# Performance work log

Hardware: AMD Instinct MI355X
Metric: run time of the kernel (lower is better)

The kernel has to match this reference:

```python
import jax, jax.numpy as jnp
import numpy as np

D = 256        # feature dim
H = 8          # num_heads
HD = D // H    # head dim = 32
G = 16         # graphs in batch
NA = 128       # nodes per graph, side A
NB = 128       # nodes per graph, side B


def setup_inputs() -> dict:
    key = jax.random.key(0)
    ks = jax.random.split(key, 7)
    s = 1.0 / np.sqrt(D)
    A = jax.random.normal(ks[0], (G * NA, D), dtype=jnp.float32)
    B = jax.random.normal(ks[1], (G * NB, D), dtype=jnp.float32)
    batch1 = jnp.repeat(jnp.arange(G, dtype=jnp.int64), NA)
    batch2 = jnp.repeat(jnp.arange(G, dtype=jnp.int64), NB)
    W1 = jax.random.normal(ks[2], (D, D), dtype=jnp.float32) * s
    bias1 = jax.random.normal(ks[3], (D,), dtype=jnp.float32) * s
    W2 = jax.random.normal(ks[4], (D, D), dtype=jnp.float32) * s
    bias2 = jax.random.normal(ks[5], (D,), dtype=jnp.float32) * s
    q = jax.random.normal(ks[6], (HD,), dtype=jnp.float32) * s
    return {"A": A, "batch1": batch1, "B": B, "batch2": batch2,
            "W1": W1, "bias1": bias1, "W2": W2, "bias2": bias2, "q": q}


def reference(A, batch1, B, batch2, W1, bias1, W2, bias2, q):
    # equal-size graphs: counts are uniform, so torch.split == reshape
    g = int(np.asarray(batch1)[-1]) + 1
    nA = A.shape[0] // g
    nB = B.shape[0] // g
    x1 = A @ W1.T + bias1            # [g*nA, D]
    x2 = B @ W2.T + bias2            # [g*nB, D]
    # faithful to torch: raw C-order view [nA, D] -> [H, nA, HD]
    x1 = x1.reshape(g, H, nA, HD)    # [g, H, nA, hd]
    x2 = x2.reshape(g, H, nB, HD)    # [g, H, nB, hd]
    # att[g,h,i,j] = sum_k tanh(x1[g,h,i,k] * x2[g,h,j,k]) * q[k]
    att = jnp.einsum('ghijk,k->ghij',
                     jnp.tanh(x1[:, :, :, None, :] * x2[:, :, None, :, :]), q)
    b2a = jax.nn.softmax(att.mean(axis=3), axis=2)   # [g, H, nA]
    a2b = jax.nn.softmax(att.mean(axis=2), axis=2)   # [g, H, nB]
    A_p = jnp.einsum('ghik,ghi->ghk', x1, b2a).reshape(g, D)
    B_p = jnp.einsum('ghjk,ghj->ghk', x2, a2b).reshape(g, D)
    return jnp.concatenate([A_p, B_p], axis=1)       # [g, 2D]
```

## Files before the change

kernel.cpp:

```cpp
#include <hip/hip_runtime.h>

#define C2L2E 2.8853900817779268f
#define LOG2E 1.4426950408889634f

#define WS_X1   0
#define WS_X2   524288
#define WS_X1S  1048576
#define WS_RS   1572864
#define WS_CQ   1589248
#define WS_AH   1703936
#define WS_AL   1966080
#define WS_BH   2228224
#define WS_BL   2490368
#define WS_W1H  2752512
#define WS_W1L  2785280
#define WS_W2H  2818048
#define WS_W2L  2850816

typedef short bf16x8 __attribute__((ext_vector_type(8)));
typedef float f32x4 __attribute__((ext_vector_type(4)));

__device__ __forceinline__ unsigned short bf16rne(float f) {
    unsigned u = __float_as_uint(f);
    u += 0x7FFF + ((u >> 16) & 1);
    return (unsigned short)(u >> 16);
}
__device__ __forceinline__ float bf16tof(unsigned short h) {
    return __uint_as_float(((unsigned)h) << 16);
}
__device__ __forceinline__ float rfl(float x) {
    return __uint_as_float(__builtin_amdgcn_readfirstlane(__float_as_uint(x)));
}

__global__ __launch_bounds__(256) void k0_convert(
        const float* __restrict__ A, const float* __restrict__ B,
        const float* __restrict__ W1, const float* __restrict__ W2,
        float* __restrict__ ws) {
    const int t = blockIdx.x * 256 + threadIdx.x;
    const float* src; unsigned short *dh, *dl; int tl;
    if (t < 65536)       { src = A;  dh = (unsigned short*)(ws + WS_AH);  dl = (unsigned short*)(ws + WS_AL);  tl = t; }
    else if (t < 131072) { src = B;  dh = (unsigned short*)(ws + WS_BH);  dl = (unsigned short*)(ws + WS_BL);  tl = t - 65536; }
    else if (t < 139264) { src = W1; dh = (unsigned short*)(ws + WS_W1H); dl = (unsigned short*)(ws + WS_W1L); tl = t - 131072; }
    else                 { src = W2; dh = (unsigned short*)(ws + WS_W2H); dl = (unsigned short*)(ws + WS_W2L); tl = t - 139264; }
    const int lane = tl & 63, kt = (tl >> 6) & 7, rt = tl >> 9;
    const int row = rt * 16 + (lane & 15);
    const int col = kt * 32 + (lane >> 4) * 8;
    float4 v0 = *(const float4*)(src + (size_t)row * 256 + col);
    float4 v1 = *(const float4*)(src + (size_t)row * 256 + col + 4);
    ushort4 h0, h1, l0, l1;
    h0.x = bf16rne(v0.x); l0.x = bf16rne(v0.x - bf16tof(h0.x));
    h0.y = bf16rne(v0.y); l0.y = bf16rne(v0.y - bf16tof(h0.y));
    h0.z = bf16rne(v0.z); l0.z = bf16rne(v0.z - bf16tof(h0.z));
    h0.w = bf16rne(v0.w); l0.w = bf16rne(v0.w - bf16tof(h0.w));
    h1.x = bf16rne(v1.x); l1.x = bf16rne(v1.x - bf16tof(h1.x));
    h1.y = bf16rne(v1.y); l1.y = bf16rne(v1.y - bf16tof(h1.y));
    h1.z = bf16rne(v1.z); l1.z = bf16rne(v1.z - bf16tof(h1.z));
    h1.w = bf16rne(v1.w); l1.w = bf16rne(v1.w - bf16tof(h1.w));
    ((ushort4*)dh)[tl * 2]     = h0;
    ((ushort4*)dh)[tl * 2 + 1] = h1;
    ((ushort4*)dl)[tl * 2]     = l0;
    ((ushort4*)dl)[tl * 2 + 1] = l1;
}

__global__ __launch_bounds__(256) void k1_mfma(
        const float* __restrict__ b1, const float* __restrict__ b2,
        float* __restrict__ ws) {
    const int bid = blockIdx.x, tid = threadIdx.x;
    const int mat = bid >> 7, idx = bid & 127;
    const int r0 = (idx >> 2) * 64, c0 = (idx & 3) * 64;
    const unsigned short* IH  = (const unsigned short*)(ws + (mat ? WS_BH : WS_AH));
    const unsigned short* IL  = (const unsigned short*)(ws + (mat ? WS_BL : WS_AL));
    const unsigned short* WHp = (const unsigned short*)(ws + (mat ? WS_W2H : WS_W1H));
    const unsigned short* WLp = (const unsigned short*)(ws + (mat ? WS_W2L : WS_W1L));
    const float* bs = mat ? b2 : b1;
    float* xo = ws + (mat ? WS_X2 : WS_X1);

    const int wv = tid >> 6, lane = tid & 63;
    const int rt = (idx >> 2) * 4 + wv;
    const int ct0 = (idx & 3) * 4;

    f32x4 acc[4];
    #pragma unroll
    for (int nt = 0; nt < 4; ++nt) acc[nt] = (f32x4){0.f, 0.f, 0.f, 0.f};

    for (int kt = 0; kt < 8; ++kt) {
        bf16x8 ah = *(const bf16x8*)(IH + ((size_t)(rt * 8 + kt) * 64 + lane) * 8);
        bf16x8 al = *(const bf16x8*)(IL + ((size_t)(rt * 8 + kt) * 64 + lane) * 8);
        #pragma unroll
        for (int nt = 0; nt < 4; ++nt) {
            const int ct = ct0 + nt;
            bf16x8 wh = *(const bf16x8*)(WHp + ((size_t)(ct * 8 + kt) * 64 + lane) * 8);
            bf16x8 wl = *(const bf16x8*)(WLp + ((size_t)(ct * 8 + kt) * 64 + lane) * 8);
            acc[nt] = __builtin_amdgcn_mfma_f32_16x16x32_bf16(ah, wh, acc[nt], 0, 0, 0);
            acc[nt] = __builtin_amdgcn_mfma_f32_16x16x32_bf16(ah, wl, acc[nt], 0, 0, 0);
            acc[nt] = __builtin_amdgcn_mfma_f32_16x16x32_bf16(al, wh, acc[nt], 0, 0, 0);
        }
    }

    const int rowb = r0 + wv * 16 + (lane >> 4) * 4;
    const int l16 = lane & 15;
    #pragma unroll
    for (int nt = 0; nt < 4; ++nt) {
        const int col = c0 + nt * 16 + l16;
        const float bb = bs[col];
        #pragma unroll
        for (int rg = 0; rg < 4; ++rg) {
            float v = acc[nt][rg] + bb;
            xo[(size_t)(rowb + rg) * 256 + col] = v;
            if (mat == 0)
                ws[WS_X1S + (size_t)(rowb + rg) * 256 + col] = v * C2L2E;
        }
    }
}

__global__ __launch_bounds__(512, 6) void k2_att(
        const float* __restrict__ x1v, const float* __restrict__ x2v,
        const float* __restrict__ q,
        float* __restrict__ rowsum, float* __restrict__ colq) {
    const int bid = blockIdx.x;
    const int gh = bid >> 2;
    const int qd = bid & 3;
    const int tid = threadIdx.x;
    const int j = tid & 127;
    const int iset = __builtin_amdgcn_readfirstlane(tid >> 7);

    __shared__ float Smat[32 * 132];
    __shared__ float colp[4][128];
    __shared__ float red8[32][8];

    float xr[32];
    {
        const float4* xp = (const float4*)(x2v + (size_t)gh * 4096 + (size_t)j * 32);
        #pragma unroll
        for (int k4 = 0; k4 < 8; ++k4) {
            float4 v = xp[k4];
            xr[k4*4+0] = v.x; xr[k4*4+1] = v.y; xr[k4*4+2] = v.z; xr[k4*4+3] = v.w;
        }
    }
    float qt[32];
    #pragma unroll
    for (int k4 = 0; k4 < 8; ++k4) {
        float4 v = *(const float4*)(q + k4 * 4);
        qt[k4*4+0] = rfl(v.x) * -2.0f;
        qt[k4*4+1] = rfl(v.y) * -2.0f;
        qt[k4*4+2] = rfl(v.z) * -2.0f;
        qt[k4*4+3] = rfl(v.w) * -2.0f;
    }

    const float* x1base = x1v + (size_t)gh * 4096 + (size_t)(qd * 32 + iset * 8) * 32;
    float colacc = 0.f;

    for (int r = 0; r < 8; ++r) {
        float a[32];
        #pragma unroll
        for (int k4 = 0; k4 < 8; ++k4) {
            float4 v = *(const float4*)(x1base + r * 32 + k4 * 4);
            a[k4*4+0] = rfl(v.x);
            a[k4*4+1] = rfl(v.y);
            a[k4*4+2] = rfl(v.z);
            a[k4*4+3] = rfl(v.w);
        }
        float S0 = 0.f, S1 = 0.f;
        #pragma unroll
        for (int kp = 0; kp < 16; ++kp) {
            float p0 = a[2*kp]   * xr[2*kp];
            float p1 = a[2*kp+1] * xr[2*kp+1];
            float d0 = __builtin_amdgcn_exp2f(fminf(p0, 60.f)) + 1.f;
            float d1 = __builtin_amdgcn_exp2f(fminf(p1, 60.f)) + 1.f;
            float rD = __builtin_amdgcn_rcpf(d0 * d1);
            float U  = fmaf(qt[2*kp+1], d0, qt[2*kp] * d1);
            if (kp & 1) S1 = fmaf(U, rD, S1); else S0 = fmaf(U, rD, S0);
        }
        float S = S0 + S1;
        colacc += S;
        Smat[(iset * 8 + r) * 132 + j] = S;
    }
    colp[iset][j] = colacc;
    __syncthreads();

    if (tid < 256) {
        const int row = tid >> 3, seg = tid & 7;
        const float4* sp = (const float4*)(Smat + row * 132 + seg * 16);
        float4 v0 = sp[0], v1 = sp[1], v2 = sp[2], v3 = sp[3];
        red8[row][seg] = (v0.x+v0.y+v0.z+v0.w) + (v1.x+v1.y+v1.z+v1.w)
                       + (v2.x+v2.y+v2.z+v2.w) + (v3.x+v3.y+v3.z+v3.w);
    }
    __syncthreads();
    if (tid < 32) {
        float s = 0.f;
        #pragma unroll
        for (int m = 0; m < 8; ++m) s += red8[tid][m];
        rowsum[gh * 128 + qd * 32 + tid] = s;
    }
    if (tid < 128) {
        colq[(size_t)bid * 128 + tid] =
            colp[0][tid] + colp[1][tid] + colp[2][tid] + colp[3][tid];
    }
}

__global__ __launch_bounds__(256) void k3_out(
        const float* __restrict__ x1v, const float* __restrict__ x2v,
        const float* __restrict__ rowsum, const float* __restrict__ colq,
        float* __restrict__ out) {
    const int gh = blockIdx.x;
    const int g = gh >> 3, h = gh & 7;
    const int tid = threadIdx.x;
    const int side = tid >> 7;
    const int u = tid & 127;
    const int w2 = (u >> 6) & 1;
    const int lane = tid & 63;

    __shared__ float warr[2][128];
    __shared__ float red[4];
    __shared__ float red2[4];
    __shared__ float part[2][4][32];

    float m;
    if (side == 0) {
        m = rowsum[gh * 128 + u] * 0.0078125f;
    } else {
        m = (colq[(size_t)(gh * 4 + 0) * 128 + u] + colq[(size_t)(gh * 4 + 1) * 128 + u] +
             colq[(size_t)(gh * 4 + 2) * 128 + u] + colq[(size_t)(gh * 4 + 3) * 128 + u]) * 0.0078125f;
    }

    float mx = m;
    #pragma unroll
    for (int s = 32; s >= 1; s >>= 1) mx = fmaxf(mx, __shfl_xor(mx, s));
    if (lane == 0) red[side * 2 + w2] = mx;
    __syncthreads();
    mx = fmaxf(red[side * 2], red[side * 2 + 1]);

    float e = __builtin_amdgcn_exp2f((m - mx) * LOG2E);
    float sm = e;
    #pragma unroll
    for (int s = 32; s >= 1; s >>= 1) sm += __shfl_xor(sm, s);
    if (lane == 0) red2[side * 2 + w2] = sm;
    __syncthreads();
    const float tot = red2[side * 2] + red2[side * 2 + 1];
    warr[side][u] = e * __builtin_amdgcn_rcpf(tot);
    __syncthreads();

    const int k = u & 31, is = u >> 5;
    const float* xt = (side ? x2v : x1v) + (size_t)gh * 4096;
    float p = 0.f;
    #pragma unroll 4
    for (int r = 0; r < 32; ++r)
        p = fmaf(xt[(is * 32 + r) * 32 + k], warr[side][is * 32 + r], p);
    part[side][is][k] = p;
    __syncthreads();
    if (u < 32) {
        float o = part[side][0][u] + part[side][1][u] + part[side][2][u] + part[side][3][u];
        out[(size_t)g * 512 + side * 256 + h * 32 + u] = o;
    }
}

extern "C" void kernel_launch(void* const* d_in, const int* in_sizes, int n_in,
                              void* d_out, int out_size, void* d_ws, size_t ws_size,
                              hipStream_t stream) {
    const float* A  = (const float*)d_in[0];
    const float* B  = (const float*)d_in[2];
    const float* W1 = (const float*)d_in[4];
    const float* b1 = (const float*)d_in[5];
    const float* W2 = (const float*)d_in[6];
    const float* b2 = (const float*)d_in[7];
    const float* q  = (const float*)d_in[8];
    float* ws  = (float*)d_ws;
    float* out = (float*)d_out;

    k0_convert<<<576, 256, 0, stream>>>(A, B, W1, W2, ws);
    k1_mfma<<<256, 256, 0, stream>>>(b1, b2, ws);
    k2_att<<<512, 512, 0, stream>>>(ws + WS_X1S, ws + WS_X2, q, ws + WS_RS, ws + WS_CQ);
    k3_out<<<128, 256, 0, stream>>>(ws + WS_X1, ws + WS_X2, ws + WS_RS, ws + WS_CQ, out);
}
```

Measured before the change: 43.85 us.

## Fuse bf16 split conversion into projection GEMM and drop scaled x1 copy

Removes the separate conversion kernel: the GEMM now loads fp32 A/B and W directly and splits them into hi/lo bf16 in registers before the MFMAs. The pre-scaled copy of x1 is no longer written; the scale factor is applied to x2 when it is loaded in the attention kernel. This saves one launch and the workspace round trip of the converted operands. In exchange, every block converts W tiles redundantly in its inner loop, which adds ALU work and register pressure.

```diff
diff --git a/kernel.cpp b/kernel.cpp
--- a/kernel.cpp
+++ b/kernel.cpp
@@ -5,17 +5,8 @@
 
 #define WS_X1   0
 #define WS_X2   524288
-#define WS_X1S  1048576
-#define WS_RS   1572864
-#define WS_CQ   1589248
-#define WS_AH   1703936
-#define WS_AL   1966080
-#define WS_BH   2228224
-#define WS_BL   2490368
-#define WS_W1H  2752512
-#define WS_W1L  2785280
-#define WS_W2H  2818048
-#define WS_W2L  2850816
+#define WS_RS   1048576
+#define WS_CQ   1064960
 
 typedef short bf16x8 __attribute__((ext_vector_type(8)));
 typedef float f32x4 __attribute__((ext_vector_type(4)));
@@ -31,85 +22,68 @@
 __device__ __forceinline__ float rfl(float x) {
     return __uint_as_float(__builtin_amdgcn_readfirstlane(__float_as_uint(x)));
 }
-
-__global__ __launch_bounds__(256) void k0_convert(
+__device__ __forceinline__ void cvt8(float4 v0, float4 v1, bf16x8* hi, bf16x8* lo) {
+    unsigned short h[8], l[8];
+    float f[8] = {v0.x, v0.y, v0.z, v0.w, v1.x, v1.y, v1.z, v1.w};
+    #pragma unroll
+    for (int e = 0; e < 8; ++e) {
+        h[e] = bf16rne(f[e]);
+        l[e] = bf16rne(f[e] - bf16tof(h[e]));
+    }
+    #pragma unroll
+    for (int e = 0; e < 8; ++e) { (*hi)[e] = (short)h[e]; (*lo)[e] = (short)l[e]; }
+}
+
+__global__ __launch_bounds__(256) void k01_gemm(
         const float* __restrict__ A, const float* __restrict__ B,
-        const float* __restrict__ W1, const float* __restrict__ W2,
-        float* __restrict__ ws) {
-    const int t = blockIdx.x * 256 + threadIdx.x;
-    const float* src; unsigned short *dh, *dl; int tl;
-    if (t < 65536)       { src = A;  dh = (unsigned short*)(ws + WS_AH);  dl = (unsigned short*)(ws + WS_AL);  tl = t; }
-    else if (t < 131072) { src = B;  dh = (unsigned short*)(ws + WS_BH);  dl = (unsigned short*)(ws + WS_BL);  tl = t - 65536; }
-    else if (t < 139264) { src = W1; dh = (unsigned short*)(ws + WS_W1H); dl = (unsigned short*)(ws + WS_W1L); tl = t - 131072; }
-    else                 { src = W2; dh = (unsigned short*)(ws + WS_W2H); dl = (unsigned short*)(ws + WS_W2L); tl = t - 139264; }
-    const int lane = tl & 63, kt = (tl >> 6) & 7, rt = tl >> 9;
-    const int row = rt * 16 + (lane & 15);
-    const int col = kt * 32 + (lane >> 4) * 8;
-    float4 v0 = *(const float4*)(src + (size_t)row * 256 + col);
-    float4 v1 = *(const float4*)(src + (size_t)row * 256 + col + 4);
-    ushort4 h0, h1, l0, l1;
-    h0.x = bf16rne(v0.x); l0.x = bf16rne(v0.x - bf16tof(h0.x));
-    h0.y = bf16rne(v0.y); l0.y = bf16rne(v0.y - bf16tof(h0.y));
-    h0.z = bf16rne(v0.z); l0.z = bf16rne(v0.z - bf16tof(h0.z));
-    h0.w = bf16rne(v0.w); l0.w = bf16rne(v0.w - bf16tof(h0.w));
-    h1.x = bf16rne(v1.x); l1.x = bf16rne(v1.x - bf16tof(h1.x));
-    h1.y = bf16rne(v1.y); l1.y = bf16rne(v1.y - bf16tof(h1.y));
-    h1.z = bf16rne(v1.z); l1.z = bf16rne(v1.z - bf16tof(h1.z));
-    h1.w = bf16rne(v1.w); l1.w = bf16rne(v1.w - bf16tof(h1.w));
-    ((ushort4*)dh)[tl * 2]     = h0;
-    ((ushort4*)dh)[tl * 2 + 1] = h1;
-    ((ushort4*)dl)[tl * 2]     = l0;
-    ((ushort4*)dl)[tl * 2 + 1] = l1;
-}
-
-__global__ __launch_bounds__(256) void k1_mfma(
-        const float* __restrict__ b1, const float* __restrict__ b2,
+        const float* __restrict__ W1, const float* __restrict__ b1,
+        const float* __restrict__ W2, const float* __restrict__ b2,
         float* __restrict__ ws) {
     const int bid = blockIdx.x, tid = threadIdx.x;
     const int mat = bid >> 7, idx = bid & 127;
     const int r0 = (idx >> 2) * 64, c0 = (idx & 3) * 64;
-    const unsigned short* IH  = (const unsigned short*)(ws + (mat ? WS_BH : WS_AH));
-    const unsigned short* IL  = (const unsigned short*)(ws + (mat ? WS_BL : WS_AL));
-    const unsigned short* WHp = (const unsigned short*)(ws + (mat ? WS_W2H : WS_W1H));
-    const unsigned short* WLp = (const unsigned short*)(ws + (mat ? WS_W2L : WS_W1L));
+    const float* In = mat ? B : A;
+    const float* Wm = mat ? W2 : W1;
     const float* bs = mat ? b2 : b1;
     float* xo = ws + (mat ? WS_X2 : WS_X1);
 
     const int wv = tid >> 6, lane = tid & 63;
-    const int rt = (idx >> 2) * 4 + wv;
-    const int ct0 = (idx & 3) * 4;
+    const int l16 = lane & 15, kbase = (lane >> 4) * 8;
+    const int arow = r0 + wv * 16 + l16;
+
+    bf16x8 ah[8], al[8];
+    #pragma unroll
+    for (int kt = 0; kt < 8; ++kt) {
+        const float* p = In + (size_t)arow * 256 + kt * 32 + kbase;
+        cvt8(*(const float4*)p, *(const float4*)(p + 4), &ah[kt], &al[kt]);
+    }
 
     f32x4 acc[4];
     #pragma unroll
     for (int nt = 0; nt < 4; ++nt) acc[nt] = (f32x4){0.f, 0.f, 0.f, 0.f};
 
+    #pragma unroll 2
     for (int kt = 0; kt < 8; ++kt) {
-        bf16x8 ah = *(const bf16x8*)(IH + ((size_t)(rt * 8 + kt) * 64 + lane) * 8);
-        bf16x8 al = *(const bf16x8*)(IL + ((size_t)(rt * 8 + kt) * 64 + lane) * 8);
         #pragma unroll
         for (int nt = 0; nt < 4; ++nt) {
-            const int ct = ct0 + nt;
-            bf16x8 wh = *(const bf16x8*)(WHp + ((size_t)(ct * 8 + kt) * 64 + lane) * 8);
-            bf16x8 wl = *(const bf16x8*)(WLp + ((size_t)(ct * 8 + kt) * 64 + lane) * 8);
-            acc[nt] = __builtin_amdgcn_mfma_f32_16x16x32_bf16(ah, wh, acc[nt], 0, 0, 0);
-            acc[nt] = __builtin_amdgcn_mfma_f32_16x16x32_bf16(ah, wl, acc[nt], 0, 0, 0);
-            acc[nt] = __builtin_amdgcn_mfma_f32_16x16x32_bf16(al, wh, acc[nt], 0, 0, 0);
+            const int wcol = c0 + nt * 16 + l16;
+            const float* p = Wm + (size_t)wcol * 256 + kt * 32 + kbase;
+            bf16x8 wh, wl;
+            cvt8(*(const float4*)p, *(const float4*)(p + 4), &wh, &wl);
+            acc[nt] = __builtin_amdgcn_mfma_f32_16x16x32_bf16(ah[kt], wh, acc[nt], 0, 0, 0);
+            acc[nt] = __builtin_amdgcn_mfma_f32_16x16x32_bf16(ah[kt], wl, acc[nt], 0, 0, 0);
+            acc[nt] = __builtin_amdgcn_mfma_f32_16x16x32_bf16(al[kt], wh, acc[nt], 0, 0, 0);
         }
     }
 
     const int rowb = r0 + wv * 16 + (lane >> 4) * 4;
-    const int l16 = lane & 15;
     #pragma unroll
     for (int nt = 0; nt < 4; ++nt) {
         const int col = c0 + nt * 16 + l16;
         const float bb = bs[col];
         #pragma unroll
-        for (int rg = 0; rg < 4; ++rg) {
-            float v = acc[nt][rg] + bb;
-            xo[(size_t)(rowb + rg) * 256 + col] = v;
-            if (mat == 0)
-                ws[WS_X1S + (size_t)(rowb + rg) * 256 + col] = v * C2L2E;
-        }
+        for (int rg = 0; rg < 4; ++rg)
+            xo[(size_t)(rowb + rg) * 256 + col] = acc[nt][rg] + bb;
     }
 }
 
@@ -134,7 +108,8 @@
         #pragma unroll
         for (int k4 = 0; k4 < 8; ++k4) {
             float4 v = xp[k4];
-            xr[k4*4+0] = v.x; xr[k4*4+1] = v.y; xr[k4*4+2] = v.z; xr[k4*4+3] = v.w;
+            xr[k4*4+0] = v.x * C2L2E; xr[k4*4+1] = v.y * C2L2E;
+            xr[k4*4+2] = v.z * C2L2E; xr[k4*4+3] = v.w * C2L2E;
         }
     }
     float qt[32];
@@ -267,8 +242,7 @@
     float* ws  = (float*)d_ws;
     float* out = (float*)d_out;
 
-    k0_convert<<<576, 256, 0, stream>>>(A, B, W1, W2, ws);
-    k1_mfma<<<256, 256, 0, stream>>>(b1, b2, ws);
-    k2_att<<<512, 512, 0, stream>>>(ws + WS_X1S, ws + WS_X2, q, ws + WS_RS, ws + WS_CQ);
+    k01_gemm<<<256, 256, 0, stream>>>(A, B, W1, b1, W2, b2, ws);
+    k2_att<<<512, 512, 0, stream>>>(ws + WS_X1, ws + WS_X2, q, ws + WS_RS, ws + WS_CQ);
     k3_out<<<128, 256, 0, stream>>>(ws + WS_X1, ws + WS_X2, ws + WS_RS, ws + WS_CQ, out);
 }
```

New measurement: 123.9 us. +182.6%, slower.
